# Kernel optimization log

Measured on AMD Instinct MI355X. Metric: run time of the kernel, lower is better.

## Reference

```python
import jax, jax.numpy as jnp
import numpy as np

N_HEADS = 16
EPS = -1e9  # masking constant from the original module


def setup_inputs() -> dict:
    key = jax.random.key(0)
    ks = jax.random.split(key, 5)
    B, S, D = 2, 2048, 1024
    x = jax.random.normal(ks[0], (B, S, D), dtype=jnp.float32)
    attention_mask = jax.random.randint(ks[1], (B, S), 0, 2, dtype=jnp.int32)
    W_qkv_kernel = jax.random.normal(ks[2], (D, 3 * D), dtype=jnp.float32) * (D ** -0.5)
    W_qkv_bias = jnp.zeros((3 * D,), dtype=jnp.float32)
    c_proj_kernel = jax.random.normal(ks[3], (D, D), dtype=jnp.float32) * (D ** -0.5)
    c_proj_bias = jnp.zeros((D,), dtype=jnp.float32)
    return {"x": x, "attention_mask": attention_mask,
            "W_qkv_kernel": W_qkv_kernel, "W_qkv_bias": W_qkv_bias,
            "c_proj_kernel": c_proj_kernel, "c_proj_bias": c_proj_bias}


def reference(x, attention_mask, W_qkv_kernel, W_qkv_bias, c_proj_kernel, c_proj_bias):
    B, S, D = x.shape
    H = N_HEADS
    Dh = D // H
    qkv = x @ W_qkv_kernel + W_qkv_bias                  # [B,S,3D]
    q, k, v = jnp.split(qkv, 3, axis=-1)
    # [B,S,D] -> [B,H,S,Dh]
    q = q.reshape(B, S, H, Dh).transpose(0, 2, 1, 3)
    k = k.reshape(B, S, H, Dh).transpose(0, 2, 1, 3)
    v = v.reshape(B, S, H, Dh).transpose(0, 2, 1, 3)
    scores = jnp.einsum('bhqd,bhkd->bhqk', q, k)          # [B,H,S,S]
    # NOTE: original applies masks BEFORE scaling; keep that order faithfully.
    pad = attention_mask[:, None, None, :] == 0           # [B,1,1,S]
    scores = jnp.where(pad, EPS, scores)
    causal = jnp.tril(jnp.ones((S, S), dtype=bool))
    scores = jnp.where(causal[None, None, :, :], scores, EPS)
    scaled = scores / jnp.sqrt(jnp.float32(Dh))
    attn = jax.nn.softmax(scaled, axis=-1)
    ctx = jnp.einsum('bhqk,bhkd->bhqd', attn, v)          # [B,H,S,Dh]
    ctx = ctx.transpose(0, 2, 1, 3).reshape(B, S, D)
    return ctx @ c_proj_kernel + c_proj_bias
```

## Files before the change

### kernel.cpp

```cpp
#include <hip/hip_runtime.h>
#include <hip/hip_bf16.h>
#include <stdint.h>

typedef __bf16 bf16_t;
typedef __bf16 bf16x4_t __attribute__((ext_vector_type(4)));
typedef __bf16 bf16x8_t __attribute__((ext_vector_type(8)));
typedef float f32x4_t __attribute__((ext_vector_type(4)));
typedef unsigned int u32x2_t __attribute__((ext_vector_type(2)));

#define S_LEN   2048
#define DMODEL  1024
#define NH      16
#define DH      64
#define LOG2E   1.4426950408889634f
#define SCL     (0.125f * LOG2E)
#define EPS2    (-1.8033688e8f)

#define MFMA(a, b, c) __builtin_amdgcn_mfma_f32_16x16x32_bf16(a, b, c, 0, 0, 0)

#define GLOAD_LDS16(gsrc, ldst)                                         \
  __builtin_amdgcn_global_load_lds(                                     \
      (__attribute__((address_space(1))) void*)(void*)(gsrc),           \
      (__attribute__((address_space(3))) void*)(void*)(ldst), 16, 0, 0)

__global__ void k_cvt_bf16(const float* __restrict__ in, bf16_t* __restrict__ out, int n4) {
  int i = blockIdx.x * blockDim.x + threadIdx.x;
  if (i >= n4) return;
  float4 v = reinterpret_cast<const float4*>(in)[i];
  bf16x4_t o = {(bf16_t)v.x, (bf16_t)v.y, (bf16_t)v.z, (bf16_t)v.w};
  reinterpret_cast<bf16x4_t*>(out)[i] = o;
}

__global__ void k_mask(const int* __restrict__ am, float* __restrict__ mskf, int n) {
  int i = blockIdx.x * blockDim.x + threadIdx.x;
  if (i < n) mskf[i] = am[i] ? 0.f : EPS2;
}

__global__ void k_transpose_bf16(const float* __restrict__ in, bf16_t* __restrict__ out,
                                 int R, int C) {
  __shared__ float tile[32][33];
  int c0 = blockIdx.x * 32, r0 = blockIdx.y * 32;
  int tx = threadIdx.x, ty = threadIdx.y;
  for (int i = ty; i < 32; i += 8)
    tile[i][tx] = in[(size_t)(r0 + i) * C + (c0 + tx)];
  __syncthreads();
  for (int i = ty; i < 32; i += 8)
    out[(size_t)(c0 + i) * R + (r0 + tx)] = (bf16_t)tile[tx][i];
}

template<int MODE>
__global__ __launch_bounds__(256, 2)
void k_gemm(const bf16_t* __restrict__ A, const bf16_t* __restrict__ Bt,
            const float* __restrict__ bias,
            bf16_t* __restrict__ Qb, bf16_t* __restrict__ Kb, bf16_t* __restrict__ Vt,
            float* __restrict__ Out, int M, int N, int K) {
  constexpr int BN  = (MODE == 0) ? 192 : 64;
  constexpr int JN  = BN / 32;
  constexpr int BST = BN / 32;
  __shared__ alignas(16) bf16_t As[2][128 * 64];
  __shared__ alignas(16) bf16_t Bs[2][BN * 64];
  const int tid = threadIdx.x;
  const int lane = tid & 63;
  const int w = tid >> 6;
  const int hl = blockIdx.y * gridDim.x + blockIdx.x;
  const int xcd = hl & 7, tt = hl >> 3;
  const int mb = ((xcd >> 1) << 3) + (tt >> 3);
  const int nb = ((xcd & 1) << 3) + (tt & 7);
  const int m0 = mb * 128;
  const int n0 = nb * BN;
  const int wm = (w >> 1) * 64, wn = (w & 1) * (BN / 2);
  const int l15 = lane & 15, lg = lane >> 4;
  const int lrow = lane >> 3;
  const int lcsw = (((lane & 7) ^ lrow) * 8);
  const int swz8 = (l15 & 7) * 8;

  f32x4_t acc[4][JN] = {};

#define GSTAGE(k0_, buf_)                                                        \
  do {                                                                           \
    _Pragma("unroll")                                                            \
    for (int p = 0; p < 4; ++p) {                                                \
      const int rb = w * 32 + p * 8;                                             \
      GLOAD_LDS16(&A[(size_t)(m0 + rb + lrow) * K + (k0_) + lcsw],               \
                  &As[buf_][rb * 64]);                                           \
    }                                                                            \
    _Pragma("unroll")                                                            \
    for (int p = 0; p < BST; ++p) {                                              \
      const int rb = w * (BST * 8) + p * 8;                                      \
      GLOAD_LDS16(&Bt[(size_t)(n0 + rb + lrow) * K + (k0_) + lcsw],              \
                  &Bs[buf_][rb * 64]);                                           \
    }                                                                            \
  } while (0)

  GSTAGE(0, 0);
  int buf = 0;
  for (int k0 = 0; k0 < K; k0 += 64) {
    if (k0 + 64 < K) {
      GSTAGE(k0 + 64, buf ^ 1);
      if (MODE == 0) asm volatile("s_waitcnt vmcnt(10)" ::: "memory");
      else           asm volatile("s_waitcnt vmcnt(6)"  ::: "memory");
    } else {
      asm volatile("s_waitcnt vmcnt(0)" ::: "memory");
    }
    __builtin_amdgcn_s_barrier();
    __builtin_amdgcn_sched_barrier(0);
    const bf16_t* Asb = As[buf];
    const bf16_t* Bsb = Bs[buf];
#pragma unroll
    for (int kk = 0; kk < 64; kk += 32) {
      bf16x8_t a[4], b[JN];
      const int kof = kk + 8 * lg;
#pragma unroll
      for (int i = 0; i < 4; ++i)
        a[i] = *reinterpret_cast<const bf16x8_t*>(
            &Asb[(wm + i * 16 + l15) * 64 + (kof ^ swz8)]);
#pragma unroll
      for (int j = 0; j < JN; ++j)
        b[j] = *reinterpret_cast<const bf16x8_t*>(
            &Bsb[(wn + j * 16 + l15) * 64 + (kof ^ swz8)]);
      __builtin_amdgcn_s_setprio(1);
#pragma unroll
      for (int i = 0; i < 4; ++i)
#pragma unroll
        for (int j = 0; j < JN; ++j)
          acc[i][j] = MFMA(a[i], b[j], acc[i][j]);
      __builtin_amdgcn_s_setprio(0);
    }
    __builtin_amdgcn_sched_barrier(0);
    __builtin_amdgcn_s_barrier();
    buf ^= 1;
  }
#undef GSTAGE

  const int rbase = lg * 4;
#pragma unroll
  for (int i = 0; i < 4; ++i)
#pragma unroll
    for (int j = 0; j < JN; ++j) {
      const int ncol = n0 + wn + j * 16 + l15;
      const float bs = bias[ncol];
      if (MODE == 1) {
#pragma unroll
        for (int r = 0; r < 4; ++r) {
          int m = m0 + wm + i * 16 + rbase + r;
          Out[(size_t)m * N + ncol] = acc[i][j][r] + bs;
        }
      } else {
        const int mrow0 = m0 + wm + i * 16 + rbase;
        const int b2 = mrow0 >> 11, s0 = mrow0 & 2047;
        const int t = ncol >> 10, nn = ncol & 1023;
        const int h = nn >> 6, d = nn & 63;
        const size_t bh = (size_t)b2 * NH + h;
        if (t == 2) {
          bf16x4_t o;
#pragma unroll
          for (int r = 0; r < 4; ++r) o[r] = (bf16_t)(acc[i][j][r] + bs);
          *reinterpret_cast<bf16x4_t*>(&Vt[(bh * DH + d) * S_LEN + s0]) = o;
        } else {
          bf16_t* dst = (t == 0 ? Qb : Kb) + (bh * S_LEN + s0) * DH + d;
#pragma unroll
          for (int r = 0; r < 4; ++r)
            dst[(size_t)r * DH] = (bf16_t)(acc[i][j][r] + bs);
        }
      }
    }
}

__global__ __launch_bounds__(256)
void k_vmean(const bf16_t* __restrict__ Vt, float* __restrict__ vmean) {
  const int bh = blockIdx.x;
  const int t = threadIdx.x;
  const int d = t >> 2, q = t & 3;
  const bf16_t* vp = Vt + ((size_t)bh * DH + d) * S_LEN + q * 512;
  float s = 0.f;
  for (int i = 0; i < 512; i += 8) {
    bf16x8_t v = *reinterpret_cast<const bf16x8_t*>(&vp[i]);
    for (int j = 0; j < 8; ++j) s += (float)v[j];
  }
  __shared__ float part[256];
  part[t] = s;
  __syncthreads();
  if (q == 0)
    vmean[bh * DH + d] = (part[t] + part[t + 1] + part[t + 2] + part[t + 3]) * (1.f / 2048.f);
}

__global__ __launch_bounds__(256, 2)
void k_attn(const bf16_t* __restrict__ Qb, const bf16_t* __restrict__ Kb,
            const bf16_t* __restrict__ Vt, const float* __restrict__ mskf,
            const float* __restrict__ vmean, bf16_t* __restrict__ ctxb) {
  __shared__ alignas(16) char smem[65536];
  const int tid = threadIdx.x, lane = tid & 63, w = tid >> 6;
  const int bh = blockIdx.x, b = bh >> 4, h = bh & 15;
  const int y = blockIdx.y;
  const int qst = (y < 8) ? (15 - 2 * y) : (2 * (y - 8));
  const int qbase = qst * 128 + w * 32;
  const int l15 = lane & 15, lg = lane >> 4;
  const int qg0 = qbase + l15, qg1 = qbase + 16 + l15;
  const bf16_t* Qp = Qb + (size_t)bh * S_LEN * DH;
  const char*   Kg = (const char*)(Kb + (size_t)bh * S_LEN * DH);
  const char*   Vg = (const char*)(Vt + (size_t)bh * DH * S_LEN);
  const float*  mp = mskf + b * S_LEN;

  const int srow = lane >> 3;
  const int scol = ((lane & 7) * 16) ^ (srow * 16);
  const int vrow = lane >> 4;
  const int swz  = 16 * (l15 & 7);

  const bf16x8_t qA0 = *reinterpret_cast<const bf16x8_t*>(&Qp[qg0 * DH + 8 * lg]);
  const bf16x8_t qA1 = *reinterpret_cast<const bf16x8_t*>(&Qp[qg0 * DH + 32 + 8 * lg]);
  const bf16x8_t qB0 = *reinterpret_cast<const bf16x8_t*>(&Qp[qg1 * DH + 8 * lg]);
  const bf16x8_t qB1 = *reinterpret_cast<const bf16x8_t*>(&Qp[qg1 * DH + 32 + 8 * lg]);

  f32x4_t poA[4] = {}, poB[4] = {};
  float lA = 0.f, lB = 0.f;

#define STAGE_PH(ph_, buf_)                                                        \
  do {                                                                             \
    const int kb_ = (ph_) * 128;                                                   \
    _Pragma("unroll")                                                              \
    for (int jj = 0; jj < 4; ++jj) {                                               \
      const int rk = w * 32 + jj * 8;                                              \
      GLOAD_LDS16(Kg + (size_t)(kb_ + rk + srow) * 128 + scol,                     \
                  smem + (buf_) * 16384 + rk * 128);                               \
      const int rv = w * 16 + jj * 4;                                              \
      const int vc = ((lane & 15) * 16) ^ ((((jj << 2) + vrow) & 7) * 16);         \
      GLOAD_LDS16(Vg + (size_t)(rv + vrow) * 4096 + (size_t)kb_ * 2 + vc,          \
                  smem + 32768 + (buf_) * 16384 + rv * 256);                       \
    }                                                                              \
  } while (0)

#define QK_SUB(S_, STA, STB)                                                       \
  _Pragma("unroll")                                                                \
  for (int t = 0; t < 4; ++t) {                                                    \
    const int rbyte = ((S_) * 64 + t * 16 + l15) * 128;                            \
    bf16x8_t k0 = *reinterpret_cast<const bf16x8_t*>(Ksb + rbyte + ((16 * lg) ^ swz));       \
    bf16x8_t k1 = *reinterpret_cast<const bf16x8_t*>(Ksb + rbyte + ((64 + 16 * lg) ^ swz));  \
    f32x4_t s = {}; s = MFMA(k0, qA0, s); s = MFMA(k1, qA1, s); STA[t] = s;        \
    f32x4_t s2 = {}; s2 = MFMA(k0, qB0, s2); s2 = MFMA(k1, qB1, s2); STB[t] = s2;  \
  }

#define SM_PACK(ST, MK, LACC, PF, QG, CAUSAL, KB0)                                 \
  do {                                                                             \
    float e[16];                                                                   \
    _Pragma("unroll")                                                              \
    for (int t = 0; t < 4; ++t)                                                    \
      _Pragma("unroll")                                                            \
      for (int r = 0; r < 4; ++r) {                                                \
        float v = fmaf(ST[t][r], SCL, MK[t][r]);                                   \
        if (CAUSAL) {                                                              \
          int k = (KB0) + t * 16 + lg * 4 + r;                                     \
          v = (k <= (QG)) ? v : EPS2;                                              \
        }                                                                          \
        float ex = exp2f(v);                                                       \
        e[t * 4 + r] = ex;                                                         \
        LACC += ex;                                                                \
      }                                                                            \
    _Pragma("unroll")                                                              \
    for (int g = 0; g < 2; ++g) {                                                  \
      union { uint32_t u2[4]; bf16x8_t v; } pk_;                                   \
      _Pragma("unroll")                                                            \
      for (int jj = 0; jj < 4; ++jj)                                               \
        asm("v_cvt_pk_bf16_f32 %0, %1, %2"                                         \
            : "=v"(pk_.u2[jj]) : "v"(e[8 * g + 2 * jj]), "v"(e[8 * g + 2 * jj + 1])); \
      PF[g] = pk_.v;                                                               \
    }                                                                              \
  } while (0)

#define PV_SUB(S_, PFA, PFB)                                                       \
  _Pragma("unroll")                                                                \
  for (int g = 0; g < 2; ++g)                                                      \
    _Pragma("unroll")                                                              \
    for (int f = 0; f < 4; ++f) {                                                  \
      const int rbyte = (f * 16 + l15) * 256;                                      \
      const int cb = (S_) * 128 + 64 * g + 8 * lg;                                 \
      u32x2_t va = *reinterpret_cast<const u32x2_t*>(Vsb + rbyte + (cb ^ swz));         \
      u32x2_t vb = *reinterpret_cast<const u32x2_t*>(Vsb + rbyte + ((cb + 32) ^ swz));  \
      union { uint32_t u2[4]; bf16x8_t v; } vv_;                                   \
      vv_.u2[0] = va[0]; vv_.u2[1] = va[1]; vv_.u2[2] = vb[0]; vv_.u2[3] = vb[1];  \
      poA[f] = MFMA(vv_.v, PFA[g], poA[f]);                                        \
      poB[f] = MFMA(vv_.v, PFB[g], poB[f]);                                        \
    }

  int buf = 0;
  STAGE_PH(0, 0);

  for (int ph = 0; ph < qst; ++ph) {
    const int kb = ph * 128;
    __syncthreads();
    STAGE_PH(ph + 1, buf ^ 1);
    const char* Ksb = smem + buf * 16384;
    const char* Vsb = smem + 32768 + buf * 16384;

    f32x4_t mk0[4], mk1[4];
#pragma unroll
    for (int t = 0; t < 4; ++t) {
      mk0[t] = *reinterpret_cast<const f32x4_t*>(&mp[kb + t * 16 + lg * 4]);
      mk1[t] = *reinterpret_cast<const f32x4_t*>(&mp[kb + 64 + t * 16 + lg * 4]);
    }

    f32x4_t stA0[4], stB0[4], stA1[4], stB1[4];
    __builtin_amdgcn_s_setprio(1);
    QK_SUB(0, stA0, stB0);
    QK_SUB(1, stA1, stB1);
    __builtin_amdgcn_s_setprio(0);

    bf16x8_t pfA[2], pfB[2];
    SM_PACK(stA0, mk0, lA, pfA, qg0, false, 0);
    SM_PACK(stB0, mk0, lB, pfB, qg1, false, 0);
    __builtin_amdgcn_s_setprio(1);
    PV_SUB(0, pfA, pfB);
    __builtin_amdgcn_s_setprio(0);
    SM_PACK(stA1, mk1, lA, pfA, qg0, false, 0);
    SM_PACK(stB1, mk1, lB, pfB, qg1, false, 0);
    __builtin_amdgcn_s_setprio(1);
    PV_SUB(1, pfA, pfB);
    __builtin_amdgcn_s_setprio(0);
    buf ^= 1;
  }

  {
    const int kb = qst * 128;
    __syncthreads();
    const char* Ksb = smem + buf * 16384;
    const char* Vsb = smem + 32768 + buf * 16384;

    f32x4_t mk0[4], mk1[4];
#pragma unroll
    for (int t = 0; t < 4; ++t) {
      mk0[t] = *reinterpret_cast<const f32x4_t*>(&mp[kb + t * 16 + lg * 4]);
      mk1[t] = *reinterpret_cast<const f32x4_t*>(&mp[kb + 64 + t * 16 + lg * 4]);
    }

    f32x4_t stA0[4], stB0[4], stA1[4], stB1[4];
    bf16x8_t pfA[2], pfB[2];
    QK_SUB(0, stA0, stB0);
    SM_PACK(stA0, mk0, lA, pfA, qg0, true, kb);
    SM_PACK(stB0, mk0, lB, pfB, qg1, true, kb);
    PV_SUB(0, pfA, pfB);
    if (w >= 2) {
      QK_SUB(1, stA1, stB1);
      SM_PACK(stA1, mk1, lA, pfA, qg0, true, kb + 64);
      SM_PACK(stB1, mk1, lB, pfB, qg1, true, kb + 64);
      PV_SUB(1, pfA, pfB);
    }
  }
#undef STAGE_PH
#undef QK_SUB
#undef SM_PACK
#undef PV_SUB

  lA += __shfl_xor(lA, 16); lA += __shfl_xor(lA, 32);
  lB += __shfl_xor(lB, 16); lB += __shfl_xor(lB, 32);
  const float* vm = vmean + bh * DH;
  {
    const bool dead = (lA == 0.f);
    const float inv = dead ? 0.f : 1.0f / lA;
    bf16_t* orow = ctxb + (size_t)(b * S_LEN + qg0) * DMODEL + h * DH;
#pragma unroll
    for (int f = 0; f < 4; ++f) {
      bf16x4_t o;
#pragma unroll
      for (int r = 0; r < 4; ++r) {
        int d = f * 16 + lg * 4 + r;
        o[r] = (bf16_t)(dead ? vm[d] : poA[f][r] * inv);
      }
      *reinterpret_cast<bf16x4_t*>(&orow[f * 16 + lg * 4]) = o;
    }
  }
  {
    const bool dead = (lB == 0.f);
    const float inv = dead ? 0.f : 1.0f / lB;
    bf16_t* orow = ctxb + (size_t)(b * S_LEN + qg1) * DMODEL + h * DH;
#pragma unroll
    for (int f = 0; f < 4; ++f) {
      bf16x4_t o;
#pragma unroll
      for (int r = 0; r < 4; ++r) {
        int d = f * 16 + lg * 4 + r;
        o[r] = (bf16_t)(dead ? vm[d] : poB[f][r] * inv);
      }
      *reinterpret_cast<bf16x4_t*>(&orow[f * 16 + lg * 4]) = o;
    }
  }
}

extern "C" void kernel_launch(void* const* d_in, const int* in_sizes, int n_in,
                              void* d_out, int out_size, void* d_ws, size_t ws_size,
                              hipStream_t stream) {
  const float* x     = (const float*)d_in[0];
  const int*   amask = (const int*)d_in[1];
  const float* Wqkv  = (const float*)d_in[2];
  const float* bqkv  = (const float*)d_in[3];
  const float* Wproj = (const float*)d_in[4];
  const float* bproj = (const float*)d_in[5];
  float* out = (float*)d_out;

  char* ws = (char*)d_ws;
  bf16_t* xb    = (bf16_t*)(ws);
  bf16_t* WqT   = (bf16_t*)(ws + (8llu  << 20));
  bf16_t* WpT   = (bf16_t*)(ws + (14llu << 20));
  bf16_t* Qb    = (bf16_t*)(ws + (16llu << 20));
  bf16_t* Kb    = (bf16_t*)(ws + (24llu << 20));
  bf16_t* Vt    = (bf16_t*)(ws + (32llu << 20));
  bf16_t* ctxb  = (bf16_t*)(ws + (40llu << 20));
  float*  vmean = (float*) (ws + (48llu << 20));
  float*  mskf  = (float*) (ws + (48llu << 20) + 65536);

  k_cvt_bf16<<<4096, 256, 0, stream>>>(x, xb, (2 * S_LEN * DMODEL) / 4);
  k_mask<<<16, 256, 0, stream>>>(amask, mskf, 2 * S_LEN);
  k_transpose_bf16<<<dim3(3072 / 32, 1024 / 32), dim3(32, 8), 0, stream>>>(Wqkv, WqT, 1024, 3072);
  k_transpose_bf16<<<dim3(1024 / 32, 1024 / 32), dim3(32, 8), 0, stream>>>(Wproj, WpT, 1024, 1024);
  k_gemm<0><<<dim3(3072 / 192, 4096 / 128), 256, 0, stream>>>(
      xb, WqT, bqkv, Qb, Kb, Vt, nullptr, 4096, 3072, 1024);
  k_vmean<<<32, 256, 0, stream>>>(Vt, vmean);
  k_attn<<<dim3(32, 16), 256, 0, stream>>>(Qb, Kb, Vt, mskf, vmean, ctxb);
  k_gemm<1><<<dim3(1024 / 64, 4096 / 128), 256, 0, stream>>>(
      ctxb, WpT, bproj, nullptr, nullptr, nullptr, out, 4096, 1024, 1024);
}
```

Baseline: 123.2 us.

## Split KV range across two warp groups and pair causal stripes per block

The attention kernel now launches 512-thread blocks with two 4-wave groups. Each group streams half of a query stripe's causal KV range into its own 64KB double-buffered LDS region. Partial outputs and row sums are merged through LDS before the epilogue. Each block handles a complementary pair of stripes (15-pr and pr), so every block gets about the same amount of causal work. The aim is a shorter critical path per stripe and better load balance, at the cost of 128KB of dynamic LDS, extra barriers and a merge step.

```diff
diff --git a/kernel.cpp b/kernel.cpp
--- a/kernel.cpp
+++ b/kernel.cpp
@@ -184,18 +184,16 @@
     vmean[bh * DH + d] = (part[t] + part[t + 1] + part[t + 2] + part[t + 3]) * (1.f / 2048.f);
 }
 
-__global__ __launch_bounds__(256, 2)
+__global__ __launch_bounds__(512, 2)
 void k_attn(const bf16_t* __restrict__ Qb, const bf16_t* __restrict__ Kb,
             const bf16_t* __restrict__ Vt, const float* __restrict__ mskf,
             const float* __restrict__ vmean, bf16_t* __restrict__ ctxb) {
-  __shared__ alignas(16) char smem[65536];
+  extern __shared__ char smem[];
   const int tid = threadIdx.x, lane = tid & 63, w = tid >> 6;
-  const int bh = blockIdx.x, b = bh >> 4, h = bh & 15;
-  const int y = blockIdx.y;
-  const int qst = (y < 8) ? (15 - 2 * y) : (2 * (y - 8));
-  const int qbase = qst * 128 + w * 32;
+  const int wg = w >> 2, wl = w & 3;
+  const int bh = blockIdx.x, b = bh >> 4, hh = bh & 15;
+  const int pr = blockIdx.y;
   const int l15 = lane & 15, lg = lane >> 4;
-  const int qg0 = qbase + l15, qg1 = qbase + 16 + l15;
   const bf16_t* Qp = Qb + (size_t)bh * S_LEN * DH;
   const char*   Kg = (const char*)(Kb + (size_t)bh * S_LEN * DH);
   const char*   Vg = (const char*)(Vt + (size_t)bh * DH * S_LEN);
@@ -205,27 +203,20 @@
   const int scol = ((lane & 7) * 16) ^ (srow * 16);
   const int vrow = lane >> 4;
   const int swz  = 16 * (l15 & 7);
-
-  const bf16x8_t qA0 = *reinterpret_cast<const bf16x8_t*>(&Qp[qg0 * DH + 8 * lg]);
-  const bf16x8_t qA1 = *reinterpret_cast<const bf16x8_t*>(&Qp[qg0 * DH + 32 + 8 * lg]);
-  const bf16x8_t qB0 = *reinterpret_cast<const bf16x8_t*>(&Qp[qg1 * DH + 8 * lg]);
-  const bf16x8_t qB1 = *reinterpret_cast<const bf16x8_t*>(&Qp[qg1 * DH + 32 + 8 * lg]);
-
-  f32x4_t poA[4] = {}, poB[4] = {};
-  float lA = 0.f, lB = 0.f;
+  char* gbase = smem + wg * 65536;
 
 #define STAGE_PH(ph_, buf_)                                                        \
   do {                                                                             \
     const int kb_ = (ph_) * 128;                                                   \
     _Pragma("unroll")                                                              \
     for (int jj = 0; jj < 4; ++jj) {                                               \
-      const int rk = w * 32 + jj * 8;                                              \
+      const int rk = wl * 32 + jj * 8;                                             \
       GLOAD_LDS16(Kg + (size_t)(kb_ + rk + srow) * 128 + scol,                     \
-                  smem + (buf_) * 16384 + rk * 128);                               \
-      const int rv = w * 16 + jj * 4;                                              \
+                  gbase + (buf_) * 16384 + rk * 128);                              \
+      const int rv = wl * 16 + jj * 4;                                             \
       const int vc = ((lane & 15) * 16) ^ ((((jj << 2) + vrow) & 7) * 16);         \
       GLOAD_LDS16(Vg + (size_t)(rv + vrow) * 4096 + (size_t)kb_ * 2 + vc,          \
-                  smem + 32768 + (buf_) * 16384 + rv * 256);                       \
+                  gbase + 32768 + (buf_) * 16384 + rv * 256);                      \
     }                                                                              \
   } while (0)
 
@@ -281,107 +272,130 @@
       poB[f] = MFMA(vv_.v, PFB[g], poB[f]);                                        \
     }
 
-  int buf = 0;
-  STAGE_PH(0, 0);
-
-  for (int ph = 0; ph < qst; ++ph) {
-    const int kb = ph * 128;
+  auto run_stripe = [&](int s) {
+    const int qbase = s * 128 + wl * 32;
+    const int qg0 = qbase + l15, qg1 = qbase + 16 + l15;
+    const bf16x8_t qA0 = *reinterpret_cast<const bf16x8_t*>(&Qp[qg0 * DH + 8 * lg]);
+    const bf16x8_t qA1 = *reinterpret_cast<const bf16x8_t*>(&Qp[qg0 * DH + 32 + 8 * lg]);
+    const bf16x8_t qB0 = *reinterpret_cast<const bf16x8_t*>(&Qp[qg1 * DH + 8 * lg]);
+    const bf16x8_t qB1 = *reinterpret_cast<const bf16x8_t*>(&Qp[qg1 * DH + 32 + 8 * lg]);
+    f32x4_t poA[4] = {}, poB[4] = {};
+    float lA = 0.f, lB = 0.f;
+    const int hs = (s + 2) >> 1;
+
     __syncthreads();
-    STAGE_PH(ph + 1, buf ^ 1);
-    const char* Ksb = smem + buf * 16384;
-    const char* Vsb = smem + 32768 + buf * 16384;
-
-    f32x4_t mk0[4], mk1[4];
-#pragma unroll
-    for (int t = 0; t < 4; ++t) {
-      mk0[t] = *reinterpret_cast<const f32x4_t*>(&mp[kb + t * 16 + lg * 4]);
-      mk1[t] = *reinterpret_cast<const f32x4_t*>(&mp[kb + 64 + t * 16 + lg * 4]);
-    }
-
-    f32x4_t stA0[4], stB0[4], stA1[4], stB1[4];
-    __builtin_amdgcn_s_setprio(1);
-    QK_SUB(0, stA0, stB0);
-    QK_SUB(1, stA1, stB1);
-    __builtin_amdgcn_s_setprio(0);
-
-    bf16x8_t pfA[2], pfB[2];
-    SM_PACK(stA0, mk0, lA, pfA, qg0, false, 0);
-    SM_PACK(stB0, mk0, lB, pfB, qg1, false, 0);
-    __builtin_amdgcn_s_setprio(1);
-    PV_SUB(0, pfA, pfB);
-    __builtin_amdgcn_s_setprio(0);
-    SM_PACK(stA1, mk1, lA, pfA, qg0, false, 0);
-    SM_PACK(stB1, mk1, lB, pfB, qg1, false, 0);
-    __builtin_amdgcn_s_setprio(1);
-    PV_SUB(1, pfA, pfB);
-    __builtin_amdgcn_s_setprio(0);
-    buf ^= 1;
-  }
-
-  {
-    const int kb = qst * 128;
+    int buf = 0;
+    if (wg == 0) STAGE_PH(0, 0);
+    else if (hs <= s) STAGE_PH(hs, 0);
+
+    for (int i = 0; i < hs; ++i) {
+      __syncthreads();
+      if (wg == 0) { if (i + 1 < hs) STAGE_PH(i + 1, buf ^ 1); }
+      else         { if (hs + i + 1 <= s) STAGE_PH(hs + i + 1, buf ^ 1); }
+      const int p = (wg == 0) ? i : hs + i;
+      if (wg == 0 || p <= s) {
+        const char* Ksb = gbase + buf * 16384;
+        const char* Vsb = gbase + 32768 + buf * 16384;
+        const int kb = p * 128;
+        f32x4_t mk0[4], mk1[4];
+#pragma unroll
+        for (int t = 0; t < 4; ++t) {
+          mk0[t] = *reinterpret_cast<const f32x4_t*>(&mp[kb + t * 16 + lg * 4]);
+          mk1[t] = *reinterpret_cast<const f32x4_t*>(&mp[kb + 64 + t * 16 + lg * 4]);
+        }
+        f32x4_t stA0[4], stB0[4], stA1[4], stB1[4];
+        bf16x8_t pfA[2], pfB[2];
+        if (p < s) {
+          __builtin_amdgcn_s_setprio(1);
+          QK_SUB(0, stA0, stB0);
+          QK_SUB(1, stA1, stB1);
+          __builtin_amdgcn_s_setprio(0);
+          SM_PACK(stA0, mk0, lA, pfA, qg0, false, 0);
+          SM_PACK(stB0, mk0, lB, pfB, qg1, false, 0);
+          __builtin_amdgcn_s_setprio(1);
+          PV_SUB(0, pfA, pfB);
+          __builtin_amdgcn_s_setprio(0);
+          SM_PACK(stA1, mk1, lA, pfA, qg0, false, 0);
+          SM_PACK(stB1, mk1, lB, pfB, qg1, false, 0);
+          __builtin_amdgcn_s_setprio(1);
+          PV_SUB(1, pfA, pfB);
+          __builtin_amdgcn_s_setprio(0);
+        } else {
+          QK_SUB(0, stA0, stB0);
+          SM_PACK(stA0, mk0, lA, pfA, qg0, true, kb);
+          SM_PACK(stB0, mk0, lB, pfB, qg1, true, kb);
+          PV_SUB(0, pfA, pfB);
+          if (wl >= 2) {
+            QK_SUB(1, stA1, stB1);
+            SM_PACK(stA1, mk1, lA, pfA, qg0, true, kb + 64);
+            SM_PACK(stB1, mk1, lB, pfB, qg1, true, kb + 64);
+            PV_SUB(1, pfA, pfB);
+          }
+        }
+      }
+      buf ^= 1;
+    }
+
     __syncthreads();
-    const char* Ksb = smem + buf * 16384;
-    const char* Vsb = smem + 32768 + buf * 16384;
-
-    f32x4_t mk0[4], mk1[4];
-#pragma unroll
-    for (int t = 0; t < 4; ++t) {
-      mk0[t] = *reinterpret_cast<const f32x4_t*>(&mp[kb + t * 16 + lg * 4]);
-      mk1[t] = *reinterpret_cast<const f32x4_t*>(&mp[kb + 64 + t * 16 + lg * 4]);
-    }
-
-    f32x4_t stA0[4], stB0[4], stA1[4], stB1[4];
-    bf16x8_t pfA[2], pfB[2];
-    QK_SUB(0, stA0, stB0);
-    SM_PACK(stA0, mk0, lA, pfA, qg0, true, kb);
-    SM_PACK(stB0, mk0, lB, pfB, qg1, true, kb);
-    PV_SUB(0, pfA, pfB);
-    if (w >= 2) {
-      QK_SUB(1, stA1, stB1);
-      SM_PACK(stA1, mk1, lA, pfA, qg0, true, kb + 64);
-      SM_PACK(stB1, mk1, lB, pfB, qg1, true, kb + 64);
-      PV_SUB(1, pfA, pfB);
-    }
-  }
+    float* mb_ = (float*)(smem + 65536) + ((size_t)wl * 64 + lane) * 36;
+    if (wg == 1) {
+#pragma unroll
+      for (int f = 0; f < 4; ++f) {
+        *reinterpret_cast<f32x4_t*>(mb_ + f * 4)      = poA[f];
+        *reinterpret_cast<f32x4_t*>(mb_ + 16 + f * 4) = poB[f];
+      }
+      mb_[32] = lA; mb_[33] = lB;
+    }
+    __syncthreads();
+    if (wg == 0) {
+#pragma unroll
+      for (int f = 0; f < 4; ++f) {
+        poA[f] += *reinterpret_cast<const f32x4_t*>(mb_ + f * 4);
+        poB[f] += *reinterpret_cast<const f32x4_t*>(mb_ + 16 + f * 4);
+      }
+      lA += mb_[32]; lB += mb_[33];
+      lA += __shfl_xor(lA, 16); lA += __shfl_xor(lA, 32);
+      lB += __shfl_xor(lB, 16); lB += __shfl_xor(lB, 32);
+      const float* vm = vmean + bh * DH;
+      {
+        const bool dead = (lA == 0.f);
+        const float inv = dead ? 0.f : 1.0f / lA;
+        bf16_t* orow = ctxb + (size_t)(b * S_LEN + qg0) * DMODEL + hh * DH;
+#pragma unroll
+        for (int f = 0; f < 4; ++f) {
+          bf16x4_t o;
+#pragma unroll
+          for (int r = 0; r < 4; ++r) {
+            int d = f * 16 + lg * 4 + r;
+            o[r] = (bf16_t)(dead ? vm[d] : poA[f][r] * inv);
+          }
+          *reinterpret_cast<bf16x4_t*>(&orow[f * 16 + lg * 4]) = o;
+        }
+      }
+      {
+        const bool dead = (lB == 0.f);
+        const float inv = dead ? 0.f : 1.0f / lB;
+        bf16_t* orow = ctxb + (size_t)(b * S_LEN + qg1) * DMODEL + hh * DH;
+#pragma unroll
+        for (int f = 0; f < 4; ++f) {
+          bf16x4_t o;
+#pragma unroll
+          for (int r = 0; r < 4; ++r) {
+            int d = f * 16 + lg * 4 + r;
+            o[r] = (bf16_t)(dead ? vm[d] : poB[f][r] * inv);
+          }
+          *reinterpret_cast<bf16x4_t*>(&orow[f * 16 + lg * 4]) = o;
+        }
+      }
+    }
+  };
+
+  run_stripe(15 - pr);
+  run_stripe(pr);
 #undef STAGE_PH
 #undef QK_SUB
 #undef SM_PACK
 #undef PV_SUB
-
-  lA += __shfl_xor(lA, 16); lA += __shfl_xor(lA, 32);
-  lB += __shfl_xor(lB, 16); lB += __shfl_xor(lB, 32);
-  const float* vm = vmean + bh * DH;
-  {
-    const bool dead = (lA == 0.f);
-    const float inv = dead ? 0.f : 1.0f / lA;
-    bf16_t* orow = ctxb + (size_t)(b * S_LEN + qg0) * DMODEL + h * DH;
-#pragma unroll
-    for (int f = 0; f < 4; ++f) {
-      bf16x4_t o;
-#pragma unroll
-      for (int r = 0; r < 4; ++r) {
-        int d = f * 16 + lg * 4 + r;
-        o[r] = (bf16_t)(dead ? vm[d] : poA[f][r] * inv);
-      }
-      *reinterpret_cast<bf16x4_t*>(&orow[f * 16 + lg * 4]) = o;
-    }
-  }
-  {
-    const bool dead = (lB == 0.f);
-    const float inv = dead ? 0.f : 1.0f / lB;
-    bf16_t* orow = ctxb + (size_t)(b * S_LEN + qg1) * DMODEL + h * DH;
-#pragma unroll
-    for (int f = 0; f < 4; ++f) {
-      bf16x4_t o;
-#pragma unroll
-      for (int r = 0; r < 4; ++r) {
-        int d = f * 16 + lg * 4 + r;
-        o[r] = (bf16_t)(dead ? vm[d] : poB[f][r] * inv);
-      }
-      *reinterpret_cast<bf16x4_t*>(&orow[f * 16 + lg * 4]) = o;
-    }
-  }
 }
 
 extern "C" void kernel_launch(void* const* d_in, const int* in_sizes, int n_in,
@@ -413,7 +427,7 @@
   k_gemm<0><<<dim3(3072 / 192, 4096 / 128), 256, 0, stream>>>(
       xb, WqT, bqkv, Qb, Kb, Vt, nullptr, 4096, 3072, 1024);
   k_vmean<<<32, 256, 0, stream>>>(Vt, vmean);
-  k_attn<<<dim3(32, 16), 256, 0, stream>>>(Qb, Kb, Vt, mskf, vmean, ctxb);
+  k_attn<<<dim3(32, 8), 512, 131072, stream>>>(Qb, Kb, Vt, mskf, vmean, ctxb);
   k_gemm<1><<<dim3(1024 / 64, 4096 / 128), 256, 0, stream>>>(
       ctxb, WpT, bproj, nullptr, nullptr, nullptr, out, 4096, 1024, 1024);
 }
```

Measured after the change: 122.6 us. About the same (-0.5%).
